# Kernel optimization log

Measured on AMD Instinct MI355X. Metric: run time of the kernel, lower is better.

The kernel has to match this reference:

```python
import jax, jax.numpy as jnp
import numpy as np
from jax import lax

N = 50000
C = 8
HW = 11
E = 800000
BD = 4
LIN_DIM = C * (HW - 2) * (HW - 2) + BD  # 652
HID = 256
OUT = 5
EPS = 1e-5


def _layernorm(h, g, b):
    mu = jnp.mean(h, axis=-1, keepdims=True)
    var = jnp.var(h, axis=-1, keepdims=True)
    return (h - mu) * lax.rsqrt(var + EPS) * g + b


def setup_inputs() -> dict:
    key = jax.random.key(0)
    ks = jax.random.split(key, 20)
    x = jax.random.normal(ks[0], (N, C, HW, HW), dtype=jnp.float32)
    bd_pred = jax.random.normal(ks[1], (N, BD), dtype=jnp.float32)
    src = jax.random.randint(ks[2], (E,), 0, N)
    dst = jax.random.randint(ks[3], (E,), 0, N)
    dst = jnp.where(src == dst, (dst + 1) % N, dst)  # no self loops
    edge_index = jnp.stack([src, dst]).astype(jnp.int64)
    s = 0.02
    p = {
        'conv_self_w': jax.random.normal(ks[4], (C, C, 3, 3), jnp.float32) * s,
        'conv_self_b': jnp.zeros((C,), jnp.float32),
        'lin_w': jax.random.normal(ks[5], (HID, LIN_DIM), jnp.float32) * s,
        'lin_b': jnp.zeros((HID,), jnp.float32),
        'lin_self_w': jax.random.normal(ks[6], (HID, LIN_DIM), jnp.float32) * s,
        'lin_self_b': jnp.zeros((HID,), jnp.float32),
        'sage_l_w': jax.random.normal(ks[7], (3, HID, HID), jnp.float32) * s,
        'sage_l_b': jnp.zeros((3, HID), jnp.float32),
        'sage_r_w': jax.random.normal(ks[8], (3, HID, HID), jnp.float32) * s,
        'ln_g': jnp.ones((2, HID), jnp.float32),
        'ln_b': jnp.zeros((2, HID), jnp.float32),
        'mp1_w': jax.random.normal(ks[9], (HID, HID), jnp.float32) * s,
        'mp1_b': jnp.zeros((HID,), jnp.float32),
        'mp2_w': jax.random.normal(ks[10], (OUT, HID), jnp.float32) * s,
        'mp2_b': jnp.zeros((OUT,), jnp.float32),
    }
    return dict(x=x, bd_pred=bd_pred, edge_index=edge_index, **p)


def reference(x, bd_pred, edge_index, conv_self_w, conv_self_b, lin_w, lin_b,
              lin_self_w, lin_self_b, sage_l_w, sage_l_b, sage_r_w,
              ln_g, ln_b, mp1_w, mp1_b, mp2_w, mp2_b):
    n = x.shape[0]
    src, dst = edge_index[0], edge_index[1]

    # CustomConv layer 0: conv_self -> flatten -> hstack(bd_pred) -> relu -> two linears
    h = lax.conv_general_dilated(x, conv_self_w, (1, 1), 'VALID',
                                 dimension_numbers=('NCHW', 'OIHW', 'NCHW'))
    h = h + conv_self_b[None, :, None, None]
    h = jnp.concatenate([h.reshape(n, -1), bd_pred], axis=1)  # [N, 652]
    h = jax.nn.relu(h)
    self_x = h @ lin_self_w.T + lin_self_b
    neigh = h @ lin_w.T + lin_b
    h = self_x + jax.ops.segment_sum(neigh[src], dst, num_segments=n)  # aggr='add'

    # in-degree for SAGEConv mean aggregation
    deg = jax.ops.segment_sum(jnp.ones((src.shape[0],), h.dtype), dst, num_segments=n)
    deg = jnp.maximum(deg, 1.0)[:, None]

    emb = h
    for i in range(3):  # SAGEConv layers 1..3
        mean_agg = jax.ops.segment_sum(h[src], dst, num_segments=n) / deg
        h = mean_agg @ sage_l_w[i].T + sage_l_b[i] + h @ sage_r_w[i].T
        emb = h
        h = jax.nn.relu(h)
        # dropout p=0.25 is identity in eval mode
        if i != 2:
            h = _layernorm(h, ln_g[i], ln_b[i])

    z = h @ mp1_w.T + mp1_b
    z = z @ mp2_w.T + mp2_b
    return emb, jax.nn.log_softmax(z, axis=1)
```

## Files before the change

kernel.cpp:

```cpp
#include <hip/hip_runtime.h>
#include <hip/hip_bf16.h>
#include <stdint.h>

#define NN 50000
#define EE 800000

typedef unsigned short u16;
typedef __attribute__((ext_vector_type(4))) float f32x4;
typedef __attribute__((ext_vector_type(8))) short bf16x8;

__device__ __forceinline__ float bu2f(u16 u){ return __uint_as_float(((unsigned)u)<<16); }
__device__ __forceinline__ u16 f2bu(float f){
  unsigned u = __float_as_uint(f);
  u += 0x7fffu + ((u>>16)&1u);
  return (u16)(u>>16);
}

__global__ void sniff_kernel(const int* __restrict__ e, const u16* __restrict__ xu,
                             int* __restrict__ flags){
  __shared__ int nz, cnt;
  int t = threadIdx.x;
  if (t == 0){ nz = 0; cnt = 0; }
  __syncthreads();
  if (e[2*t + 1] != 0) atomicOr(&nz, 1);
  u16 u = xu[2*t];
  int ef = (u >> 7) & 0xFF;
  int ok = (u == 0) || (ef >= 118 && ef <= 132);
  atomicAdd(&cnt, ok);
  __syncthreads();
  if (t == 0){ flags[0] = (nz == 0) ? 1 : 0; flags[1] = (cnt >= 200) ? 1 : 0; }
}

__global__ void convert_edges_kernel(const void* __restrict__ ep, int* __restrict__ outp,
                                     const int* __restrict__ flags, int total){
  int i = blockIdx.x*256 + threadIdx.x;
  if (i >= total) return;
  if (flags[0]) outp[i] = (int)((const long long*)ep)[i];
  else          outp[i] = ((const int*)ep)[i];
}

struct CanonTab {
  const void* src[15];
  void*       dst[15];
  int rows[15];
  int sk[15];
  int dk[15];
  int tobf[15];
};

__global__ __launch_bounds__(256) void canon_params_kernel(CanonTab tab, const int* __restrict__ flags){
  int a = blockIdx.y;
  int isbf = flags[1];
  int rows = tab.rows[a], sk = tab.sk[a], dk = tab.dk[a], tobf = tab.tobf[a];
  int n = rows * dk;
  int base = (blockIdx.x*256 + threadIdx.x) * 8;
  if (base >= n) return;
  #pragma unroll
  for (int uu = 0; uu < 8; uu++){
    int i = base + uu;
    if (i >= n) break;
    int r = i / dk, c = i - r*dk;
    float v = 0.f;
    if (c < sk){
      size_t si = (size_t)r*sk + c;
      v = isbf ? bu2f(((const u16*)tab.src[a])[si]) : ((const float*)tab.src[a])[si];
    }
    if (tobf) ((u16*)tab.dst[a])[i] = f2bu(v);
    else      ((float*)tab.dst[a])[i] = v;
  }
}

__global__ __launch_bounds__(256) void conv_relu_kernel(
    const void* __restrict__ xraw, const void* __restrict__ bdraw,
    const float* __restrict__ cw, const float* __restrict__ cb,
    const int* __restrict__ flags, u16* __restrict__ h0){
  __shared__ float xs[968];
  __shared__ float wsm[576];
  __shared__ float bs[8];
  int n = blockIdx.x, t = threadIdx.x;
  int isbf = flags[1];
  if (isbf){
    const ushort4* xp = (const ushort4*)((const u16*)xraw + (size_t)n*968);
    if (t < 242){ ushort4 u = xp[t]; xs[4*t]=bu2f(u.x); xs[4*t+1]=bu2f(u.y); xs[4*t+2]=bu2f(u.z); xs[4*t+3]=bu2f(u.w); }
  } else {
    const float4* xp = (const float4*)((const float*)xraw + (size_t)n*968);
    if (t < 242){ float4 u = xp[t]; xs[4*t]=u.x; xs[4*t+1]=u.y; xs[4*t+2]=u.z; xs[4*t+3]=u.w; }
  }
  if (t < 144){ float4 u = ((const float4*)cw)[t]; wsm[4*t]=u.x; wsm[4*t+1]=u.y; wsm[4*t+2]=u.z; wsm[4*t+3]=u.w; }
  if (t < 8) bs[t] = cb[t];
  __syncthreads();
  u16* outr = h0 + (size_t)n*704;
  if (t < 216){
    int co = t & 7;
    int rowid = t >> 3;
    int oi = rowid / 3;
    int og = rowid - oi*3;
    float wreg[72];
    #pragma unroll
    for (int q = 0; q < 72; q++) wreg[q] = wsm[co*72 + q];
    float a0 = bs[co], a1 = a0, a2 = a0;
    #pragma unroll
    for (int ci = 0; ci < 8; ci++){
      #pragma unroll
      for (int ki = 0; ki < 3; ki++){
        const float* xb = xs + ci*121 + (oi+ki)*11 + og*3;
        float x0=xb[0], x1=xb[1], x2=xb[2], x3=xb[3], x4=xb[4];
        float w0=wreg[ci*9+ki*3+0], w1=wreg[ci*9+ki*3+1], w2=wreg[ci*9+ki*3+2];
        a0 += x0*w0 + x1*w1 + x2*w2;
        a1 += x1*w0 + x2*w1 + x3*w2;
        a2 += x2*w0 + x3*w1 + x4*w2;
      }
    }
    int colbase = co*81 + oi*9 + og*3;
    outr[colbase+0] = f2bu(fmaxf(a0, 0.f));
    outr[colbase+1] = f2bu(fmaxf(a1, 0.f));
    outr[colbase+2] = f2bu(fmaxf(a2, 0.f));
  } else if (t < 220){
    int jj = t - 216;
    float v = isbf ? bu2f(((const u16*)bdraw)[(size_t)n*4 + jj]) : ((const float*)bdraw)[(size_t)n*4 + jj];
    outr[648 + jj] = f2bu(fmaxf(v, 0.f));
  } else {
    for (int c = 652 + (t - 220); c < 704; c += 36) outr[c] = 0;
  }
}

__global__ void deg_kernel(const int* __restrict__ dst, int* __restrict__ degI, int E){
  int e = blockIdx.x*256 + threadIdx.x;
  if (e < E) atomicAdd(&degI[dst[e]], 1);
}
__global__ void invdeg_kernel(const int* __restrict__ degI, float* __restrict__ inv, int n){
  int i = blockIdx.x*256 + threadIdx.x;
  if (i < n){ int d = degI[i]; inv[i] = 1.0f / (float)(d > 1 ? d : 1); }
}

__global__ __launch_bounds__(1024) void scan_kernel(const int* __restrict__ degI,
                                                    int* __restrict__ rowptr,
                                                    int* __restrict__ cursor, int n){
  __shared__ int warp_sums[16];
  __shared__ int carry;
  int t = threadIdx.x;
  if (t == 0) carry = 0;
  __syncthreads();
  for (int base = 0; base < n; base += 1024){
    int i = base + t;
    int v = (i < n) ? degI[i] : 0;
    int s = v;
    #pragma unroll
    for (int off = 1; off < 64; off <<= 1){ int u = __shfl_up(s, off); if ((t & 63) >= off) s += u; }
    if ((t & 63) == 63) warp_sums[t >> 6] = s;
    __syncthreads();
    if (t < 16){
      int wsv = warp_sums[t];
      #pragma unroll
      for (int off = 1; off < 16; off <<= 1){ int u = __shfl_up(wsv, off); if (t >= off) wsv += u; }
      warp_sums[t] = wsv;
    }
    __syncthreads();
    int block_off = (t >= 64) ? warp_sums[(t >> 6) - 1] : 0;
    int excl = carry + block_off + s - v;
    if (i < n){ rowptr[i] = excl; cursor[i] = excl; }
    int total = warp_sums[15];
    __syncthreads();
    if (t == 0) carry += total;
    __syncthreads();
  }
  if (t == 0) rowptr[n] = carry;
}

__global__ void bucket_kernel(const int* __restrict__ esrc, const int* __restrict__ edst,
                              int* __restrict__ cursor, int* __restrict__ ebuc, int E){
  int e = blockIdx.x*256 + threadIdx.x;
  if (e < E){ int pos = atomicAdd(&cursor[edst[e]], 1); ebuc[pos] = esrc[e]; }
}

__global__ __launch_bounds__(256) void gather_agg_kernel(
    const u16* __restrict__ src_feat, const u16* __restrict__ addbase,
    const float* __restrict__ scale, u16* __restrict__ outp,
    const int* __restrict__ rowptr, const int* __restrict__ ebuc){
  int wid = threadIdx.x >> 6, lane = threadIdx.x & 63;
  int n = blockIdx.x*4 + wid;
  if (n >= NN) return;
  int beg = rowptr[n], end = rowptr[n+1];
  float a0=0.f,a1=0.f,a2=0.f,a3=0.f;
  float b0=0.f,b1=0.f,b2=0.f,b3=0.f;
  int j = beg;
  for (; j + 1 < end; j += 2){
    int s0 = ebuc[j], s1 = ebuc[j+1];
    ushort4 v0 = *(const ushort4*)(src_feat + (size_t)s0*256 + lane*4);
    ushort4 v1 = *(const ushort4*)(src_feat + (size_t)s1*256 + lane*4);
    a0 += bu2f(v0.x); a1 += bu2f(v0.y); a2 += bu2f(v0.z); a3 += bu2f(v0.w);
    b0 += bu2f(v1.x); b1 += bu2f(v1.y); b2 += bu2f(v1.z); b3 += bu2f(v1.w);
  }
  if (j < end){
    ushort4 v0 = *(const ushort4*)(src_feat + (size_t)ebuc[j]*256 + lane*4);
    a0 += bu2f(v0.x); a1 += bu2f(v0.y); a2 += bu2f(v0.z); a3 += bu2f(v0.w);
  }
  float sc = scale ? scale[n] : 1.f;
  a0 = (a0+b0)*sc; a1 = (a1+b1)*sc; a2 = (a2+b2)*sc; a3 = (a3+b3)*sc;
  if (addbase){
    ushort4 b = *(const ushort4*)(addbase + (size_t)n*256 + lane*4);
    a0 += bu2f(b.x); a1 += bu2f(b.y); a2 += bu2f(b.z); a3 += bu2f(b.w);
  }
  ushort4 o; o.x = f2bu(a0); o.y = f2bu(a1); o.z = f2bu(a2); o.w = f2bu(a3);
  *(ushort4*)(outp + (size_t)n*256 + lane*4) = o;
}

__global__ __launch_bounds__(256) void gemm_mfma_kernel(
    const u16* __restrict__ A1, int lda1, const u16* __restrict__ W1, int K1,
    const u16* __restrict__ A2, int lda2, const u16* __restrict__ W2, int K2,
    const float* __restrict__ bias,
    u16* __restrict__ out_bf,
    void* __restrict__ out_emb,
    u16* __restrict__ out_relu_bf,
    const int* __restrict__ flags, int M){
  __shared__ u16 Asm[128][72];
  __shared__ u16 Wsm[128][72];
  int t = threadIdx.x;
  int wave = t >> 6, lane = t & 63;
  int wr = wave >> 1, wc = wave & 1;
  int m0 = blockIdx.x << 7;
  int o0 = blockIdx.y << 7;
  int lrow = t >> 1;
  int lk8  = (t & 1) << 3;
  int fr = lane & 15;
  int fkb = (lane >> 4) << 3;
  f32x4 acc[4][4] = {};

  for (int pass = 0; pass < 2; ++pass){
    const u16* A; const u16* W; int K, lda;
    if (pass == 0){ A = A1; W = W1; K = K1; lda = lda1; }
    else { if (!A2) break; A = A2; W = W2; K = K2; lda = lda2; }
    for (int k0 = 0; k0 < K; k0 += 64){
      int gm = m0 + lrow;
      int4 av0 = make_int4(0,0,0,0), av1 = av0, av2 = av0, av3 = av0;
      if (gm < M){
        const int4* ap = (const int4*)(A + (size_t)gm*lda + k0 + lk8);
        av0 = ap[0]; av1 = ap[2]; av2 = ap[4]; av3 = ap[6];
      }
      const int4* wp = (const int4*)(W + (size_t)(o0 + lrow)*K + k0 + lk8);
      int4 wv0 = wp[0], wv1 = wp[2], wv2 = wp[4], wv3 = wp[6];
      *(int4*)&Asm[lrow][lk8]      = av0;
      *(int4*)&Asm[lrow][lk8+16]   = av1;
      *(int4*)&Asm[lrow][lk8+32]   = av2;
      *(int4*)&Asm[lrow][lk8+48]   = av3;
      *(int4*)&Wsm[lrow][lk8]      = wv0;
      *(int4*)&Wsm[lrow][lk8+16]   = wv1;
      *(int4*)&Wsm[lrow][lk8+32]   = wv2;
      *(int4*)&Wsm[lrow][lk8+48]   = wv3;
      __syncthreads();
      #pragma unroll
      for (int kk = 0; kk < 2; kk++){
        int fk = kk*32 + fkb;
        bf16x8 af[4], wf[4];
        #pragma unroll
        for (int i = 0; i < 4; i++) af[i] = *(const bf16x8*)&Asm[wr*64 + i*16 + fr][fk];
        #pragma unroll
        for (int jj = 0; jj < 4; jj++) wf[jj] = *(const bf16x8*)&Wsm[wc*64 + jj*16 + fr][fk];
        #pragma unroll
        for (int i = 0; i < 4; i++)
          #pragma unroll
          for (int jj = 0; jj < 4; jj++)
            acc[i][jj] = __builtin_amdgcn_mfma_f32_16x16x32_bf16(af[i], wf[jj], acc[i][jj], 0, 0, 0);
      }
      __syncthreads();
    }
  }
  int isbf = flags[1];
  int fg = lane >> 4;
  #pragma unroll
  for (int i = 0; i < 4; i++){
    int rbase = m0 + wr*64 + i*16 + fg*4;
    #pragma unroll
    for (int jj = 0; jj < 4; jj++){
      int col = o0 + wc*64 + jj*16 + fr;
      float bv = bias[col];
      #pragma unroll
      for (int r = 0; r < 4; r++){
        int row = rbase + r;
        if (row < M){
          float v = acc[i][jj][r] + bv;
          size_t off = (size_t)row*256 + col;
          if (out_bf)   out_bf[off] = f2bu(v);
          if (out_emb){
            if (isbf) ((u16*)out_emb)[off] = f2bu(v);
            else      ((float*)out_emb)[off] = v;
          }
          if (out_relu_bf) out_relu_bf[off] = f2bu(fmaxf(v, 0.f));
        }
      }
    }
  }
}

__global__ __launch_bounds__(256) void relu_ln_kernel(
    const u16* __restrict__ inb, u16* __restrict__ outb,
    const float* __restrict__ g, const float* __restrict__ b){
  __shared__ float rs[4], rs2[4];
  int n = blockIdx.x, t = threadIdx.x;
  float v = fmaxf(bu2f(inb[(size_t)n*256 + t]), 0.f);
  float s = v, s2 = v*v;
  #pragma unroll
  for (int off = 1; off < 64; off <<= 1){ s += __shfl_xor(s, off); s2 += __shfl_xor(s2, off); }
  if ((t & 63) == 0){ rs[t>>6] = s; rs2[t>>6] = s2; }
  __syncthreads();
  float S  = rs[0]+rs[1]+rs[2]+rs[3];
  float S2 = rs2[0]+rs2[1]+rs2[2]+rs2[3];
  float mu  = S * (1.f/256.f);
  float var = S2 * (1.f/256.f) - mu*mu;
  float inv = rsqrtf(var + 1e-5f);
  outb[(size_t)n*256 + t] = f2bu((v - mu) * inv * g[t] + b[t]);
}

__global__ __launch_bounds__(256) void head_kernel(
    const u16* __restrict__ z1, const float* __restrict__ w2, const float* __restrict__ b2,
    void* __restrict__ outbase, size_t out_off, const int* __restrict__ flags, int M){
  __shared__ float wsm[1280];
  __shared__ float bs[5];
  int t = threadIdx.x;
  for (int i = t; i < 320; i += 256){
    float4 u = ((const float4*)w2)[i];
    wsm[4*i]=u.x; wsm[4*i+1]=u.y; wsm[4*i+2]=u.z; wsm[4*i+3]=u.w;
  }
  if (t < 5) bs[t] = b2[t];
  __syncthreads();
  int n = blockIdx.x*256 + t;
  if (n >= M) return;
  const u16* zp = z1 + (size_t)n*256;
  float acc[5];
  #pragma unroll
  for (int o = 0; o < 5; o++) acc[o] = bs[o];
  for (int k = 0; k < 256; k += 4){
    ushort4 zu = *(const ushort4*)(zp + k);
    float z0 = bu2f(zu.x), z1f = bu2f(zu.y), z2 = bu2f(zu.z), z3 = bu2f(zu.w);
    #pragma unroll
    for (int o = 0; o < 5; o++){
      const float* w = wsm + o*256 + k;
      acc[o] += z0*w[0] + z1f*w[1] + z2*w[2] + z3*w[3];
    }
  }
  float mx = acc[0];
  #pragma unroll
  for (int o = 1; o < 5; o++) mx = fmaxf(mx, acc[o]);
  float se = 0.f;
  #pragma unroll
  for (int o = 0; o < 5; o++) se += expf(acc[o] - mx);
  float lse = mx + logf(se);
  int isbf = flags[1];
  if (isbf){
    u16* op = (u16*)outbase + out_off + (size_t)n*5;
    #pragma unroll
    for (int o = 0; o < 5; o++) op[o] = f2bu(acc[o] - lse);
  } else {
    float* op = (float*)outbase + out_off + (size_t)n*5;
    #pragma unroll
    for (int o = 0; o < 5; o++) op[o] = acc[o] - lse;
  }
}

extern "C" void kernel_launch(void* const* d_in, const int* in_sizes, int n_in,
                              void* d_out, int out_size, void* d_ws, size_t ws_size,
                              hipStream_t stream){
  (void)in_sizes; (void)n_in; (void)out_size; (void)ws_size;
  const void* x    = d_in[0];
  const void* bd   = d_in[1];
  const void* eraw = d_in[2];

  char* ws = (char*)d_ws;
  const size_t OFF_H0 = 0;
  const size_t OFF_A  = OFF_H0 + (size_t)NN*704*2;
  const size_t OFF_B  = OFF_A  + (size_t)NN*256*2;
  const size_t OFF_C  = OFF_B  + (size_t)NN*256*2;
  const size_t OFF_DEG= OFF_C  + (size_t)NN*256*2;
  const size_t OFF_INV= OFF_DEG + (size_t)NN*4;
  const size_t OFF_EDG= OFF_INV + (size_t)NN*4;
  const size_t OFF_RP = OFF_EDG + (size_t)2*EE*4;
  const size_t OFF_CUR= OFF_RP  + (size_t)(NN+16)*4;
  const size_t OFF_EBU= OFF_CUR + (size_t)NN*4;
  const size_t OFF_FLG= OFF_EBU + (size_t)EE*4;
  const size_t OFF_PRM= OFF_FLG + 256;

  u16*   h0   = (u16*)(ws + OFF_H0);
  u16*   bufA = (u16*)(ws + OFF_A);
  u16*   bufB = (u16*)(ws + OFF_B);
  u16*   bufC = (u16*)(ws + OFF_C);
  int*   degI = (int*)(ws + OFF_DEG);
  float* invd = (float*)(ws + OFF_INV);
  int*   edg  = (int*)(ws + OFF_EDG);
  int*   rowp = (int*)(ws + OFF_RP);
  int*   curs = (int*)(ws + OFF_CUR);
  int*   ebuc = (int*)(ws + OFF_EBU);
  int*   flg  = (int*)(ws + OFF_FLG);
  char*  prm  = ws + OFF_PRM;
  const int* esrc = edg;
  const int* edst = edg + EE;

  static const int crows[15] = {1,1,256,1,256,1,1,1,1,1,1,1,1,1,1};
  static const int csk[15]   = {576,8,652,256,652,256,196608,768,196608,512,512,65536,256,1280,5};
  static const int cdk[15]   = {576,8,704,256,704,256,196608,768,196608,512,512,65536,256,1280,5};
  static const int ctobf[15] = {0,0,1,0,1,0,1,0,1,0,0,1,0,0,0};
  CanonTab tab;
  size_t po = 0;
  void* dsts[15];
  for (int i = 0; i < 15; i++){
    tab.src[i] = d_in[3+i];
    tab.rows[i] = crows[i]; tab.sk[i] = csk[i]; tab.dk[i] = cdk[i]; tab.tobf[i] = ctobf[i];
    dsts[i] = prm + po;
    tab.dst[i] = dsts[i];
    size_t bytes = (size_t)crows[i]*cdk[i] * (ctobf[i] ? 2 : 4);
    po += (bytes + 63) & ~(size_t)63;
  }
  const float* c_cw  = (const float*)dsts[0];
  const float* c_cb  = (const float*)dsts[1];
  const u16*   c_lw  = (const u16*)dsts[2];
  const float* c_lb  = (const float*)dsts[3];
  const u16*   c_lsw = (const u16*)dsts[4];
  const float* c_lsb = (const float*)dsts[5];
  const u16*   c_slw = (const u16*)dsts[6];
  const float* c_slb = (const float*)dsts[7];
  const u16*   c_srw = (const u16*)dsts[8];
  const float* c_lng = (const float*)dsts[9];
  const float* c_lnb = (const float*)dsts[10];
  const u16*   c_m1w = (const u16*)dsts[11];
  const float* c_m1b = (const float*)dsts[12];
  const float* c_m2w = (const float*)dsts[13];
  const float* c_m2b = (const float*)dsts[14];

  hipMemsetAsync(degI, 0, (size_t)NN*4, stream);
  sniff_kernel<<<1, 256, 0, stream>>>((const int*)eraw, (const u16*)x, flg);
  {
    dim3 cgrid(96, 15);
    canon_params_kernel<<<cgrid, 256, 0, stream>>>(tab, flg);
  }
  convert_edges_kernel<<<(2*EE + 255)/256, 256, 0, stream>>>(eraw, edg, flg, 2*EE);
  conv_relu_kernel<<<NN, 256, 0, stream>>>(x, bd, c_cw, c_cb, flg, h0);
  deg_kernel<<<(EE + 255)/256, 256, 0, stream>>>(edst, degI, EE);
  invdeg_kernel<<<(NN + 255)/256, 256, 0, stream>>>(degI, invd, NN);
  scan_kernel<<<1, 1024, 0, stream>>>(degI, rowp, curs, NN);
  bucket_kernel<<<(EE + 255)/256, 256, 0, stream>>>(esrc, edst, curs, ebuc, EE);

  dim3 ggrid((NN + 127)/128, 2);
  const int agrid = (NN + 3)/4;
  gemm_mfma_kernel<<<ggrid, 256, 0, stream>>>(h0, 704, c_lsw, 704,
      nullptr, 0, nullptr, 0, c_lsb, bufA, nullptr, nullptr, flg, NN);
  gemm_mfma_kernel<<<ggrid, 256, 0, stream>>>(h0, 704, c_lw, 704,
      nullptr, 0, nullptr, 0, c_lb, bufB, nullptr, nullptr, flg, NN);
  gather_agg_kernel<<<agrid, 256, 0, stream>>>(bufB, bufA, nullptr, bufA, rowp, ebuc);

  for (int i = 0; i < 3; i++){
    gather_agg_kernel<<<agrid, 256, 0, stream>>>(bufA, nullptr, invd, bufC, rowp, ebuc);
    const u16*   L  = c_slw + (size_t)i*256*256;
    const float* Lb = c_slb + (size_t)i*256;
    const u16*   R  = c_srw + (size_t)i*256*256;
    if (i < 2){
      gemm_mfma_kernel<<<ggrid, 256, 0, stream>>>(bufC, 256, L, 256,
          bufA, 256, R, 256, Lb, bufB, nullptr, nullptr, flg, NN);
      relu_ln_kernel<<<NN, 256, 0, stream>>>(bufB, bufA,
          c_lng + (size_t)i*256, c_lnb + (size_t)i*256);
    } else {
      gemm_mfma_kernel<<<ggrid, 256, 0, stream>>>(bufC, 256, L, 256,
          bufA, 256, R, 256, Lb, nullptr, d_out, bufB, flg, NN);
    }
  }
  gemm_mfma_kernel<<<ggrid, 256, 0, stream>>>(bufB, 256, c_m1w, 256,
      nullptr, 0, nullptr, 0, c_m1b, bufC, nullptr, nullptr, flg, NN);
  head_kernel<<<(NN + 255)/256, 256, 0, stream>>>(bufC, c_m2w, c_m2b,
      d_out, (size_t)NN*256, flg, NN);
}
```

Measured before the change: 899.8 us.

## Fuse first-layer GEMMs, widen gather loads, and vectorize the degree scan

The two first-layer linears (self and neighbour) become one 512-wide GEMM over concatenated weights, so the 704-wide h0 is read once instead of twice; the output goes into a 512-stride buffer. The gather-aggregate kernel now splits each wave into two halves that take alternate edges and load 16 bytes per lane, then combines the halves with a cross-half shuffle. The single-block prefix scan processes 8 elements per thread to cut loop iterations. In exchange, the parameter buffer layout grows and the strided gather reads half-rows from a wider buffer.

```diff
diff --git a/kernel.cpp b/kernel.cpp
--- a/kernel.cpp
+++ b/kernel.cpp
@@ -15,6 +15,8 @@
   u += 0x7fffu + ((u>>16)&1u);
   return (u16)(u>>16);
 }
+__device__ __forceinline__ float lo16f(unsigned u){ return __uint_as_float(u << 16); }
+__device__ __forceinline__ float hi16f(unsigned u){ return __uint_as_float(u & 0xffff0000u); }
 
 __global__ void sniff_kernel(const int* __restrict__ e, const u16* __restrict__ xu,
                              int* __restrict__ flags){
@@ -141,13 +143,15 @@
   int t = threadIdx.x;
   if (t == 0) carry = 0;
   __syncthreads();
-  for (int base = 0; base < n; base += 1024){
-    int i = base + t;
-    int v = (i < n) ? degI[i] : 0;
-    int s = v;
-    #pragma unroll
-    for (int off = 1; off < 64; off <<= 1){ int u = __shfl_up(s, off); if ((t & 63) >= off) s += u; }
-    if ((t & 63) == 63) warp_sums[t >> 6] = s;
+  for (int base = 0; base < n; base += 8192){
+    int i0 = base + t*8;
+    int v[8]; int s = 0;
+    #pragma unroll
+    for (int q = 0; q < 8; q++){ int idx = i0+q; v[q] = (idx < n) ? degI[idx] : 0; s += v[q]; }
+    int ts = s;
+    #pragma unroll
+    for (int off = 1; off < 64; off <<= 1){ int u = __shfl_up(ts, off); if ((t & 63) >= off) ts += u; }
+    if ((t & 63) == 63) warp_sums[t >> 6] = ts;
     __syncthreads();
     if (t < 16){
       int wsv = warp_sums[t];
@@ -156,9 +160,14 @@
       warp_sums[t] = wsv;
     }
     __syncthreads();
-    int block_off = (t >= 64) ? warp_sums[(t >> 6) - 1] : 0;
-    int excl = carry + block_off + s - v;
-    if (i < n){ rowptr[i] = excl; cursor[i] = excl; }
+    int blk = (t >= 64) ? warp_sums[(t >> 6) - 1] : 0;
+    int excl = carry + blk + ts - s;
+    #pragma unroll
+    for (int q = 0; q < 8; q++){
+      int idx = i0+q;
+      if (idx < n){ rowptr[idx] = excl; cursor[idx] = excl; }
+      excl += v[q];
+    }
     int total = warp_sums[15];
     __syncthreads();
     if (t == 0) carry += total;
@@ -174,41 +183,66 @@
 }
 
 __global__ __launch_bounds__(256) void gather_agg_kernel(
-    const u16* __restrict__ src_feat, const u16* __restrict__ addbase,
+    const u16* __restrict__ src_feat, int s_stride,
+    const u16* __restrict__ addbase, int a_stride,
     const float* __restrict__ scale, u16* __restrict__ outp,
     const int* __restrict__ rowptr, const int* __restrict__ ebuc){
   int wid = threadIdx.x >> 6, lane = threadIdx.x & 63;
   int n = blockIdx.x*4 + wid;
   if (n >= NN) return;
+  int half = lane >> 5;
+  int sub  = lane & 31;
+  int c0 = sub * 8;
   int beg = rowptr[n], end = rowptr[n+1];
-  float a0=0.f,a1=0.f,a2=0.f,a3=0.f;
-  float b0=0.f,b1=0.f,b2=0.f,b3=0.f;
-  int j = beg;
-  for (; j + 1 < end; j += 2){
-    int s0 = ebuc[j], s1 = ebuc[j+1];
-    ushort4 v0 = *(const ushort4*)(src_feat + (size_t)s0*256 + lane*4);
-    ushort4 v1 = *(const ushort4*)(src_feat + (size_t)s1*256 + lane*4);
-    a0 += bu2f(v0.x); a1 += bu2f(v0.y); a2 += bu2f(v0.z); a3 += bu2f(v0.w);
-    b0 += bu2f(v1.x); b1 += bu2f(v1.y); b2 += bu2f(v1.z); b3 += bu2f(v1.w);
-  }
-  if (j < end){
-    ushort4 v0 = *(const ushort4*)(src_feat + (size_t)ebuc[j]*256 + lane*4);
-    a0 += bu2f(v0.x); a1 += bu2f(v0.y); a2 += bu2f(v0.z); a3 += bu2f(v0.w);
-  }
-  float sc = scale ? scale[n] : 1.f;
-  a0 = (a0+b0)*sc; a1 = (a1+b1)*sc; a2 = (a2+b2)*sc; a3 = (a3+b3)*sc;
-  if (addbase){
-    ushort4 b = *(const ushort4*)(addbase + (size_t)n*256 + lane*4);
-    a0 += bu2f(b.x); a1 += bu2f(b.y); a2 += bu2f(b.z); a3 += bu2f(b.w);
-  }
-  ushort4 o; o.x = f2bu(a0); o.y = f2bu(a1); o.z = f2bu(a2); o.w = f2bu(a3);
-  *(ushort4*)(outp + (size_t)n*256 + lane*4) = o;
+  float acc[8] = {0.f,0.f,0.f,0.f,0.f,0.f,0.f,0.f};
+  int j = beg + half;
+  for (; j + 2 < end; j += 4){
+    int s0 = ebuc[j], s1 = ebuc[j+2];
+    uint4 u0 = *(const uint4*)(src_feat + (size_t)s0*s_stride + c0);
+    uint4 u1 = *(const uint4*)(src_feat + (size_t)s1*s_stride + c0);
+    acc[0] += lo16f(u0.x); acc[1] += hi16f(u0.x);
+    acc[2] += lo16f(u0.y); acc[3] += hi16f(u0.y);
+    acc[4] += lo16f(u0.z); acc[5] += hi16f(u0.z);
+    acc[6] += lo16f(u0.w); acc[7] += hi16f(u0.w);
+    acc[0] += lo16f(u1.x); acc[1] += hi16f(u1.x);
+    acc[2] += lo16f(u1.y); acc[3] += hi16f(u1.y);
+    acc[4] += lo16f(u1.z); acc[5] += hi16f(u1.z);
+    acc[6] += lo16f(u1.w); acc[7] += hi16f(u1.w);
+  }
+  for (; j < end; j += 2){
+    int s0 = ebuc[j];
+    uint4 u0 = *(const uint4*)(src_feat + (size_t)s0*s_stride + c0);
+    acc[0] += lo16f(u0.x); acc[1] += hi16f(u0.x);
+    acc[2] += lo16f(u0.y); acc[3] += hi16f(u0.y);
+    acc[4] += lo16f(u0.z); acc[5] += hi16f(u0.z);
+    acc[6] += lo16f(u0.w); acc[7] += hi16f(u0.w);
+  }
+  #pragma unroll
+  for (int q = 0; q < 8; q++) acc[q] += __shfl_xor(acc[q], 32);
+  if (half == 0){
+    float sc = scale ? scale[n] : 1.f;
+    #pragma unroll
+    for (int q = 0; q < 8; q++) acc[q] *= sc;
+    if (addbase){
+      uint4 b = *(const uint4*)(addbase + (size_t)n*a_stride + c0);
+      acc[0] += lo16f(b.x); acc[1] += hi16f(b.x);
+      acc[2] += lo16f(b.y); acc[3] += hi16f(b.y);
+      acc[4] += lo16f(b.z); acc[5] += hi16f(b.z);
+      acc[6] += lo16f(b.w); acc[7] += hi16f(b.w);
+    }
+    uint4 o;
+    o.x = (unsigned)f2bu(acc[0]) | ((unsigned)f2bu(acc[1]) << 16);
+    o.y = (unsigned)f2bu(acc[2]) | ((unsigned)f2bu(acc[3]) << 16);
+    o.z = (unsigned)f2bu(acc[4]) | ((unsigned)f2bu(acc[5]) << 16);
+    o.w = (unsigned)f2bu(acc[6]) | ((unsigned)f2bu(acc[7]) << 16);
+    *(uint4*)(outp + (size_t)n*256 + c0) = o;
+  }
 }
 
 __global__ __launch_bounds__(256) void gemm_mfma_kernel(
     const u16* __restrict__ A1, int lda1, const u16* __restrict__ W1, int K1,
     const u16* __restrict__ A2, int lda2, const u16* __restrict__ W2, int K2,
-    const float* __restrict__ bias,
+    const float* __restrict__ bias, int ldc,
     u16* __restrict__ out_bf,
     void* __restrict__ out_emb,
     u16* __restrict__ out_relu_bf,
@@ -279,7 +313,7 @@
         int row = rbase + r;
         if (row < M){
           float v = acc[i][jj][r] + bv;
-          size_t off = (size_t)row*256 + col;
+          size_t off = (size_t)row*ldc + col;
           if (out_bf)   out_bf[off] = f2bu(v);
           if (out_emb){
             if (isbf) ((u16*)out_emb)[off] = f2bu(v);
@@ -383,6 +417,7 @@
   u16*   bufA = (u16*)(ws + OFF_A);
   u16*   bufB = (u16*)(ws + OFF_B);
   u16*   bufC = (u16*)(ws + OFF_C);
+  u16*   bufAB= (u16*)(ws + OFF_B);
   int*   degI = (int*)(ws + OFF_DEG);
   float* invd = (float*)(ws + OFF_INV);
   int*   edg  = (int*)(ws + OFF_EDG);
@@ -409,12 +444,15 @@
     size_t bytes = (size_t)crows[i]*cdk[i] * (ctobf[i] ? 2 : 4);
     po += (bytes + 63) & ~(size_t)63;
   }
+  u16*   c_l2w = (u16*)dsts[4];
+  float* c_l2b = (float*)(prm + po);  po += 512*4;
+  tab.dst[2] = c_l2w + (size_t)256*704;
+  tab.dst[3] = c_l2b + 256;
+  tab.dst[5] = c_l2b;
+  po += (size_t)256*704*2;
+
   const float* c_cw  = (const float*)dsts[0];
   const float* c_cb  = (const float*)dsts[1];
-  const u16*   c_lw  = (const u16*)dsts[2];
-  const float* c_lb  = (const float*)dsts[3];
-  const u16*   c_lsw = (const u16*)dsts[4];
-  const float* c_lsb = (const float*)dsts[5];
   const u16*   c_slw = (const u16*)dsts[6];
   const float* c_slb = (const float*)dsts[7];
   const u16*   c_srw = (const u16*)dsts[8];
@@ -425,6 +463,19 @@
   const float* c_m2w = (const float*)dsts[13];
   const float* c_m2b = (const float*)dsts[14];
 
+  {
+    u16* fresh_w = (u16*)(prm + po);
+    po += (size_t)512*704*2;
+    float* fresh_b = (float*)(prm + po);
+    po += 512*4 + 64;
+    tab.dst[4] = fresh_w;
+    tab.dst[2] = fresh_w + (size_t)256*704;
+    tab.dst[5] = fresh_b;
+    tab.dst[3] = fresh_b + 256;
+    c_l2w = fresh_w;
+    c_l2b = fresh_b;
+  }
+
   hipMemsetAsync(degI, 0, (size_t)NN*4, stream);
   sniff_kernel<<<1, 256, 0, stream>>>((const int*)eraw, (const u16*)x, flg);
   {
@@ -439,30 +490,31 @@
   bucket_kernel<<<(EE + 255)/256, 256, 0, stream>>>(esrc, edst, curs, ebuc, EE);
 
   dim3 ggrid((NN + 127)/128, 2);
+  dim3 ggrid0((NN + 127)/128, 4);
   const int agrid = (NN + 3)/4;
-  gemm_mfma_kernel<<<ggrid, 256, 0, stream>>>(h0, 704, c_lsw, 704,
-      nullptr, 0, nullptr, 0, c_lsb, bufA, nullptr, nullptr, flg, NN);
-  gemm_mfma_kernel<<<ggrid, 256, 0, stream>>>(h0, 704, c_lw, 704,
-      nullptr, 0, nullptr, 0, c_lb, bufB, nullptr, nullptr, flg, NN);
-  gather_agg_kernel<<<agrid, 256, 0, stream>>>(bufB, bufA, nullptr, bufA, rowp, ebuc);
+  gemm_mfma_kernel<<<ggrid0, 256, 0, stream>>>(h0, 704, c_l2w, 704,
+      nullptr, 0, nullptr, 0, c_l2b, 512, bufAB, nullptr, nullptr, flg, NN);
+  gather_agg_kernel<<<agrid, 256, 0, stream>>>(bufAB + 256, 512, bufAB, 512,
+      nullptr, bufA, rowp, ebuc);
 
   for (int i = 0; i < 3; i++){
-    gather_agg_kernel<<<agrid, 256, 0, stream>>>(bufA, nullptr, invd, bufC, rowp, ebuc);
+    gather_agg_kernel<<<agrid, 256, 0, stream>>>(bufA, 256, nullptr, 0,
+        invd, bufC, rowp, ebuc);
     const u16*   L  = c_slw + (size_t)i*256*256;
     const float* Lb = c_slb + (size_t)i*256;
     const u16*   R  = c_srw + (size_t)i*256*256;
     if (i < 2){
       gemm_mfma_kernel<<<ggrid, 256, 0, stream>>>(bufC, 256, L, 256,
-          bufA, 256, R, 256, Lb, bufB, nullptr, nullptr, flg, NN);
+          bufA, 256, R, 256, Lb, 256, bufB, nullptr, nullptr, flg, NN);
       relu_ln_kernel<<<NN, 256, 0, stream>>>(bufB, bufA,
           c_lng + (size_t)i*256, c_lnb + (size_t)i*256);
     } else {
       gemm_mfma_kernel<<<ggrid, 256, 0, stream>>>(bufC, 256, L, 256,
-          bufA, 256, R, 256, Lb, nullptr, d_out, bufB, flg, NN);
+          bufA, 256, R, 256, Lb, 256, nullptr, d_out, bufB, flg, NN);
     }
   }
   gemm_mfma_kernel<<<ggrid, 256, 0, stream>>>(bufB, 256, c_m1w, 256,
-      nullptr, 0, nullptr, 0, c_m1b, bufC, nullptr, nullptr, flg, NN);
+      nullptr, 0, nullptr, 0, c_m1b, 256, bufC, nullptr, nullptr, flg, NN);
   head_kernel<<<(NN + 255)/256, 256, 0, stream>>>(bufC, c_m2w, c_m2b,
       d_out, (size_t)NN*256, flg, NN);
 }
```

New measurement: 877.6 us. -2.5%, faster.
